# Optimization experiments

Measured on AMD Instinct MI355X. Metric: run time of the kernel, lower is better.

Reference implementation:

```python
import jax, jax.numpy as jnp
import numpy as np

B, S, D = 4, 2048, 1024
H, K = 16, 64
EPS = 1e-3  # Keras LayerNormalization default epsilon


def setup_inputs() -> dict:
    key = jax.random.key(0)
    ks = jax.random.split(key, 11)
    s = 0.02
    return {
        "x":  jax.random.normal(ks[0], (B, S, D), jnp.float32),
        "Wq": jax.random.normal(ks[1], (D, H, K), jnp.float32) * s,
        "bq": jnp.zeros((H, K), jnp.float32),
        "Wk": jax.random.normal(ks[2], (D, H, K), jnp.float32) * s,
        "bk": jnp.zeros((H, K), jnp.float32),
        "Wv": jax.random.normal(ks[3], (D, H, K), jnp.float32) * s,
        "bv": jnp.zeros((H, K), jnp.float32),
        "Wo": jax.random.normal(ks[4], (H, K, D), jnp.float32) * s,
        "bo": jnp.zeros((D,), jnp.float32),
        "gamma": jnp.ones((D,), jnp.float32),
        "beta":  jnp.zeros((D,), jnp.float32),
    }


def reference(x, Wq, bq, Wk, bk, Wv, bv, Wo, bo, gamma, beta):
    # QKV projections (Keras MHA einsum form): [B,S,D] -> [B,S,H,K]
    q = jnp.einsum("bsd,dhk->bshk", x, Wq) + bq
    k = jnp.einsum("bsd,dhk->bshk", x, Wk) + bk
    v = jnp.einsum("bsd,dhk->bshk", x, Wv) + bv
    scale = 1.0 / jnp.sqrt(jnp.asarray(K, x.dtype))
    scores = jnp.einsum("bqhk,bshk->bhqs", q, k) * scale  # [B,H,S,S]
    attn = jax.nn.softmax(scores, axis=-1)
    ctx = jnp.einsum("bhqs,bshk->bqhk", attn, v)           # [B,S,H,K]
    attn_out = jnp.einsum("bqhk,hkd->bqd", ctx, Wo) + bo   # [B,S,D]
    # residual + LayerNorm (over last axis)
    y = x + attn_out
    mu = jnp.mean(y, axis=-1, keepdims=True)
    var = jnp.mean(jnp.square(y - mu), axis=-1, keepdims=True)
    return (y - mu) * jax.lax.rsqrt(var + EPS) * gamma + beta
```

## Files before the change

kernel.cpp:

```cpp
#include <hip/hip_runtime.h>

typedef float f32x4 __attribute__((ext_vector_type(4)));
typedef float f32x16 __attribute__((ext_vector_type(16)));
typedef __bf16 bf16x8 __attribute__((ext_vector_type(8)));
typedef __bf16 bf16x4 __attribute__((ext_vector_type(4)));
typedef __bf16 bf16x2 __attribute__((ext_vector_type(2)));
typedef unsigned short us4 __attribute__((ext_vector_type(4)));

#define DEV __device__ __forceinline__

DEV unsigned short f2bf(float f) {
  union { float f; unsigned int u; } v; v.f = f;
  unsigned int u = v.u;
  return (unsigned short)((u + 0x7FFFu + ((u >> 16) & 1u)) >> 16);
}

typedef const __attribute__((address_space(1))) void* gvp;
typedef __attribute__((address_space(3))) void* lvp;

DEV void gll16(const void* g, void* l) {
  __builtin_amdgcn_global_load_lds((gvp)g, (lvp)l, 16, 0, 0);
}

DEV float fexp2(float x) { return __builtin_amdgcn_exp2f(x); }

DEV void plswap(unsigned& a, unsigned& b) {
  asm("v_permlane32_swap_b32 %0, %1" : "+v"(a), "+v"(b));
}
DEV float xhalf_max(float v) {
  union { float f; unsigned u; } a, b;
  a.f = v; b.f = v;
  plswap(a.u, b.u);
  return fmaxf(a.f, b.f);
}
DEV float xhalf_sum(float v) {
  union { float f; unsigned u; } a, b;
  a.f = v; b.f = v;
  plswap(a.u, b.u);
  return a.f + b.f;
}

__global__ void k_convert(const float* __restrict__ in, unsigned short* __restrict__ out, int n4) {
  int i = blockIdx.x * blockDim.x + threadIdx.x;
  if (i < n4) {
    float4 v = ((const float4*)in)[i];
    us4 o = { f2bf(v.x), f2bf(v.y), f2bf(v.z), f2bf(v.w) };
    ((us4*)out)[i] = o;
  }
}

__global__ void k_transpose4(const float* __restrict__ w0, const float* __restrict__ w1,
                             const float* __restrict__ w2, const float* __restrict__ w3,
                             unsigned short* __restrict__ o0, unsigned short* __restrict__ o1,
                             unsigned short* __restrict__ o2, unsigned short* __restrict__ o3) {
  const float* in = (blockIdx.z == 0) ? w0 : (blockIdx.z == 1) ? w1 : (blockIdx.z == 2) ? w2 : w3;
  unsigned short* out = (blockIdx.z == 0) ? o0 : (blockIdx.z == 1) ? o1 : (blockIdx.z == 2) ? o2 : o3;
  __shared__ float tile[32][33];
  const int bx = blockIdx.x * 32, by = blockIdx.y * 32;
  const int tx = threadIdx.x, ty = threadIdx.y;
#pragma unroll
  for (int r = 0; r < 4; ++r)
    tile[ty + r * 8][tx] = in[(size_t)(by + ty + r * 8) * 1024 + bx + tx];
  __syncthreads();
#pragma unroll
  for (int r = 0; r < 4; ++r)
    out[(size_t)(bx + ty + r * 8) * 1024 + by + tx] = f2bf(tile[tx][ty + r * 8]);
}

template<int MODE>
__global__ void k_gemm(const unsigned short* __restrict__ A,
                       const unsigned short* __restrict__ Bt,
                       const float* __restrict__ bias,
                       void* __restrict__ outp,
                       const float* __restrict__ xres,
                       int Kd, float scale) {
  __shared__ unsigned short As[128 * 64];
  __shared__ unsigned short Bs[128 * 64];
  const int tid = threadIdx.x;
  const int lane = tid & 63;
  const int wave = tid >> 6;
  const int l15 = lane & 15;
  const int lq  = lane >> 4;
  const int wm = wave >> 1, wn = wave & 1;
  const int mbase = blockIdx.x * 128;
  const int nbase = blockIdx.y * 128;

  f32x4 acc[4][4] = {};

  for (int kt = 0; kt < Kd; kt += 64) {
    __syncthreads();
#pragma unroll
    for (int c = 0; c < 4; ++c) {
      int e = (c * 256 + tid) * 8;
      int row = e >> 6;
      int o2 = (e * 2) ^ ((row & 7) << 4);
      int col = (o2 >> 1) & 63;
      gll16(A + (size_t)(mbase + row) * Kd + kt + col,
            As + (c * 256 + (tid & ~63)) * 8);
    }
#pragma unroll
    for (int c = 0; c < 4; ++c) {
      int e = (c * 256 + tid) * 8;
      int row = e >> 6;
      int o2 = (e * 2) ^ ((row & 7) << 4);
      int col = (o2 >> 1) & 63;
      gll16(Bt + (size_t)(nbase + row) * Kd + kt + col,
            Bs + (c * 256 + (tid & ~63)) * 8);
    }
    __syncthreads();
#pragma unroll
    for (int ks = 0; ks < 2; ++ks) {
      bf16x8 af[4], bfv[4];
#pragma unroll
      for (int i = 0; i < 4; ++i) {
        int row = wm * 64 + i * 16 + l15;
        int off = row * 128 + ((((ks << 2) | lq) ^ (row & 7)) << 4);
        af[i] = *(const bf16x8*)((const char*)As + off);
      }
#pragma unroll
      for (int j = 0; j < 4; ++j) {
        int row = wn * 64 + j * 16 + l15;
        int off = row * 128 + ((((ks << 2) | lq) ^ (row & 7)) << 4);
        bfv[j] = *(const bf16x8*)((const char*)Bs + off);
      }
#pragma unroll
      for (int i = 0; i < 4; ++i)
#pragma unroll
        for (int j = 0; j < 4; ++j)
          acc[i][j] = __builtin_amdgcn_mfma_f32_16x16x32_bf16(af[i], bfv[j], acc[i][j], 0, 0, 0);
    }
  }

#pragma unroll
  for (int i = 0; i < 4; ++i) {
#pragma unroll
    for (int j = 0; j < 4; ++j) {
#pragma unroll
      for (int r = 0; r < 4; ++r) {
        int mi = mbase + wm * 64 + i * 16 + lq * 4 + r;
        int nj = nbase + wn * 64 + j * 16 + l15;
        float v = acc[i][j][r];
        if constexpr (MODE == 0) {
          v = (v + bias[nj]) * scale;
          int b = mi >> 11, s = mi & 2047, h = nj >> 6, kk = nj & 63;
          ((unsigned short*)outp)[(((size_t)((b << 4) + h) * 2048 + s) << 6) + kk] = f2bf(v);
        } else if constexpr (MODE == 1) {
          v = v + bias[mi];
          int h = mi >> 6, d = mi & 63, b = nj >> 11, s = nj & 2047;
          ((unsigned short*)outp)[(((size_t)((b << 4) + h) << 6) + d) * 2048 + s] = f2bf(v);
        } else {
          size_t idx = (size_t)mi * 1024 + nj;
          ((float*)outp)[idx] = v + bias[nj] + xres[idx];
        }
      }
    }
  }
}

__global__ __launch_bounds__(256, 4) void k_attn(const unsigned short* __restrict__ q,
                       const unsigned short* __restrict__ k,
                       const unsigned short* __restrict__ vt,
                       unsigned short* __restrict__ ctx) {
  __shared__ unsigned short KV[2][2][64 * 64];

  const int tid = threadIdx.x;
  const int lane = tid & 63;
  const int wave = tid >> 6;
  const int l31 = lane & 31;
  const int l5 = lane >> 5;

  const int bid = blockIdx.x;
  const int swz = (bid & 7) * 128 + (bid >> 3);
  const int bh = swz >> 4;
  const int qtile = swz & 15;
  const int qbase = qtile * 128;
  const size_t sl = (size_t)bh << 17;

  const int qrow = qbase + wave * 32 + l31;
  bf16x8 qreg[4];
#pragma unroll
  for (int ds = 0; ds < 4; ++ds)
    qreg[ds] = *(const bf16x8*)(q + sl + (size_t)qrow * 64 + ds * 16 + l5 * 8);

#define STAGE_KV(BUF, TT) do {                                                 \
    const int kvb_ = (TT) * 64;                                                \
    _Pragma("unroll")                                                          \
    for (int c = 0; c < 2; ++c) {                                              \
      int e = (c * 256 + tid) * 8;                                             \
      int row_ = e >> 6;                                                       \
      int o2 = (e * 2) ^ ((row_ & 7) << 4);                                    \
      int col_ = (o2 >> 1) & 63;                                               \
      gll16(k + sl + (size_t)(kvb_ + row_) * 64 + col_,                        \
            KV[BUF][0] + (c * 256 + (tid & ~63)) * 8);                         \
      gll16(vt + sl + (size_t)row_ * 2048 + kvb_ + col_,                       \
            KV[BUF][1] + (c * 256 + (tid & ~63)) * 8);                         \
    }                                                                          \
  } while (0)

  STAGE_KV(0, 0);
  __syncthreads();

  f32x16 acc0 = {}, acc1 = {};
  float mrow = -1e30f, lrow = 0.f;

  for (int t = 0; t < 32; ++t) {
    const int cur = t & 1;
    if (t < 31) STAGE_KV(cur ^ 1, t + 1);

    const char* Ksc = (const char*)KV[cur][0];
    const char* Vtc = (const char*)KV[cur][1];

    f32x16 st0 = {}, st1 = {};
    __builtin_amdgcn_s_setprio(1);
#pragma unroll
    for (int kvh = 0; kvh < 2; ++kvh) {
      bf16x8 kf[4];
#pragma unroll
      for (int ds = 0; ds < 4; ++ds) {
        int row = kvh * 32 + l31;
        kf[ds] = *(const bf16x8*)(Ksc + row * 128 + (((ds * 32 + l5 * 16)) ^ ((row & 7) << 4)));
      }
      if (kvh == 0) {
#pragma unroll
        for (int ds = 0; ds < 4; ++ds)
          st0 = __builtin_amdgcn_mfma_f32_32x32x16_bf16(kf[ds], qreg[ds], st0, 0, 0, 0);
      } else {
#pragma unroll
        for (int ds = 0; ds < 4; ++ds)
          st1 = __builtin_amdgcn_mfma_f32_32x32x16_bf16(kf[ds], qreg[ds], st1, 0, 0, 0);
      }
    }
    __builtin_amdgcn_s_setprio(0);

    float tmax[8];
#pragma unroll
    for (int i = 0; i < 8; ++i) tmax[i] = fmaxf(st0[i], st0[i + 8]);
#pragma unroll
    for (int i = 0; i < 8; ++i) tmax[i] = fmaxf(tmax[i], fmaxf(st1[i], st1[i + 8]));
    float tm = fmaxf(fmaxf(fmaxf(tmax[0], tmax[1]), fmaxf(tmax[2], tmax[3])),
                     fmaxf(fmaxf(tmax[4], tmax[5]), fmaxf(tmax[6], tmax[7])));
    tm = xhalf_max(tm);

    if (!__all(tm <= mrow + 10.0f)) {
      float mnew = fmaxf(mrow, tm);
      float alpha = fexp2(mrow - mnew);
      acc0 *= alpha;
      acc1 *= alpha;
      lrow *= alpha;
      mrow = mnew;
    }
    const float mc = mrow;

    unsigned pk0[8], pk1[8];
    float rs0 = 0.f, rs1 = 0.f, rs2 = 0.f, rs3 = 0.f;
#pragma unroll
    for (int m = 0; m < 8; ++m) {
      float a0 = fexp2(st0[2 * m] - mc), a1 = fexp2(st0[2 * m + 1] - mc);
      float b0 = fexp2(st1[2 * m] - mc), b1 = fexp2(st1[2 * m + 1] - mc);
      rs0 += a0; rs1 += a1; rs2 += b0; rs3 += b1;
      union { bf16x2 v; unsigned u; } ua, ub;
      ua.v = bf16x2{ (__bf16)a0, (__bf16)a1 };
      ub.v = bf16x2{ (__bf16)b0, (__bf16)b1 };
      pk0[m] = ua.u; pk1[m] = ub.u;
    }
    lrow += (rs0 + rs1) + (rs2 + rs3);

    bf16x8 av[2][4];
#pragma unroll
    for (int kvg = 0; kvg < 4; ++kvg)
#pragma unroll
      for (int dh = 0; dh < 2; ++dh) {
        int row = dh * 32 + l31;
        av[dh][kvg] = *(const bf16x8*)(Vtc + row * 128 + ((kvg * 32 + l5 * 16) ^ ((row & 7) << 4)));
      }

    union PF { unsigned u[4]; bf16x8 v; };
    PF pf[2][2];
#pragma unroll
    for (int kvh = 0; kvh < 2; ++kvh) {
      unsigned* pk = kvh ? pk1 : pk0;
#pragma unroll
      for (int g = 0; g < 2; ++g)
#pragma unroll
        for (int j = 0; j < 2; ++j) {
          unsigned a = pk[4 * g + j], b = pk[4 * g + 2 + j];
          plswap(a, b);
          pf[kvh][g].u[j] = a;
          pf[kvh][g].u[2 + j] = b;
        }
    }

    __builtin_amdgcn_s_setprio(1);
#pragma unroll
    for (int kvh = 0; kvh < 2; ++kvh)
#pragma unroll
      for (int g = 0; g < 2; ++g) {
        const int kvg = 2 * kvh + g;
        acc0 = __builtin_amdgcn_mfma_f32_32x32x16_bf16(av[0][kvg], pf[kvh][g].v, acc0, 0, 0, 0);
        acc1 = __builtin_amdgcn_mfma_f32_32x32x16_bf16(av[1][kvg], pf[kvh][g].v, acc1, 0, 0, 0);
      }
    __builtin_amdgcn_s_setprio(0);

    __syncthreads();
  }

  float inv = 1.f / xhalf_sum(lrow);

  unsigned short* TR = (unsigned short*)KV;
  const int qloc = wave * 32 + l31;
  const int swq = (qloc & 7) << 4;
#pragma unroll
  for (int dh = 0; dh < 2; ++dh) {
    const f32x16& ac = dh ? acc1 : acc0;
#pragma unroll
    for (int g3 = 0; g3 < 4; ++g3) {
      bf16x4 o4 = { (__bf16)(ac[4 * g3] * inv), (__bf16)(ac[4 * g3 + 1] * inv),
                    (__bf16)(ac[4 * g3 + 2] * inv), (__bf16)(ac[4 * g3 + 3] * inv) };
      *(bf16x4*)((char*)TR + qloc * 128 + ((dh * 64 + g3 * 16 + l5 * 8) ^ swq)) = o4;
    }
  }
  __syncthreads();

  const int b = bh >> 4, h = bh & 15;
  {
    int row = tid >> 1, half = tid & 1;
    int sw = (row & 7) << 4;
    unsigned short* gdst = ctx + (size_t)(b * 2048 + qbase + row) * 1024 + h * 64 + half * 32;
#pragma unroll
    for (int i = 0; i < 4; ++i) {
      bf16x8 vv = *(const bf16x8*)((const char*)TR + row * 128 + ((half * 64 + i * 16) ^ sw));
      *(bf16x8*)(gdst + i * 8) = vv;
    }
  }
#undef STAGE_KV
}

__global__ void k_ln(const float* __restrict__ y, const float* __restrict__ gamma,
                     const float* __restrict__ beta, float* __restrict__ out) {
  const int row = blockIdx.x;
  const int tid = threadIdx.x;
  const float4 v = ((const float4*)(y + (size_t)row * 1024))[tid];
  float sum = v.x + v.y + v.z + v.w;
  float sq = v.x * v.x + v.y * v.y + v.z * v.z + v.w * v.w;
#pragma unroll
  for (int m = 1; m <= 32; m <<= 1) {
    sum += __shfl_xor(sum, m);
    sq  += __shfl_xor(sq, m);
  }
  __shared__ float s1[4], s2[4];
  const int wv = tid >> 6, lane = tid & 63;
  if (lane == 0) { s1[wv] = sum; s2[wv] = sq; }
  __syncthreads();
  sum = s1[0] + s1[1] + s1[2] + s1[3];
  sq  = s2[0] + s2[1] + s2[2] + s2[3];
  const float mu = sum * (1.f / 1024.f);
  const float rs = rsqrtf(sq * (1.f / 1024.f) - mu * mu + 1e-3f);
  const float4 g  = ((const float4*)gamma)[tid];
  const float4 bb = ((const float4*)beta)[tid];
  float4 o;
  o.x = (v.x - mu) * rs * g.x + bb.x;
  o.y = (v.y - mu) * rs * g.y + bb.y;
  o.z = (v.z - mu) * rs * g.z + bb.z;
  o.w = (v.w - mu) * rs * g.w + bb.w;
  ((float4*)(out + (size_t)row * 1024))[tid] = o;
}

extern "C" void kernel_launch(void* const* d_in, const int* in_sizes, int n_in,
                              void* d_out, int out_size, void* d_ws, size_t ws_size,
                              hipStream_t stream) {
  const float* x  = (const float*)d_in[0];
  const float* Wq = (const float*)d_in[1];
  const float* bq = (const float*)d_in[2];
  const float* Wk = (const float*)d_in[3];
  const float* bk = (const float*)d_in[4];
  const float* Wv = (const float*)d_in[5];
  const float* bv = (const float*)d_in[6];
  const float* Wo = (const float*)d_in[7];
  const float* bo = (const float*)d_in[8];
  const float* gamma = (const float*)d_in[9];
  const float* beta  = (const float*)d_in[10];
  float* out = (float*)d_out;

  char* ws = (char*)d_ws;
  const size_t MB = 1024 * 1024;
  unsigned short* xb  = (unsigned short*)(ws);
  unsigned short* wqt = (unsigned short*)(ws + 16 * MB);
  unsigned short* wkt = (unsigned short*)(ws + 18 * MB);
  unsigned short* wvt = (unsigned short*)(ws + 20 * MB);
  unsigned short* wot = (unsigned short*)(ws + 22 * MB);
  unsigned short* qb  = (unsigned short*)(ws + 24 * MB);
  unsigned short* kb  = (unsigned short*)(ws + 40 * MB);
  unsigned short* vtb = (unsigned short*)(ws + 56 * MB);
  unsigned short* ctx = (unsigned short*)(ws + 72 * MB);
  float* yb = (float*)(ws + 24 * MB);

  k_convert<<<8192, 256, 0, stream>>>(x, xb, 2097152);
  dim3 tb(32, 8), tg(32, 32, 4);
  k_transpose4<<<tg, tb, 0, stream>>>(Wq, Wk, Wv, Wo, wqt, wkt, wvt, wot);

  k_gemm<0><<<dim3(64, 8), 256, 0, stream>>>(xb, wqt, bq, qb, nullptr, 1024, 0.18033688011112042f);
  k_gemm<0><<<dim3(64, 8), 256, 0, stream>>>(xb, wkt, bk, kb, nullptr, 1024, 1.0f);
  k_gemm<1><<<dim3(8, 64), 256, 0, stream>>>(wvt, xb, bv, vtb, nullptr, 1024, 1.0f);

  k_attn<<<1024, 256, 0, stream>>>(qb, kb, vtb, ctx);

  k_gemm<2><<<dim3(64, 8), 256, 0, stream>>>(ctx, wot, bo, yb, x, 1024, 1.0f);

  k_ln<<<8192, 256, 0, stream>>>(yb, gamma, beta, out);
  (void)in_sizes; (void)n_in; (void)out_size; (void)ws_size;
}
```

Measured before the change: 208.0 us.

## Double attention query tile per block and merge QKV GEMMs into one launch

The attention kernel now handles 256 query rows per block, with each wave owning two 32-row query groups that share the same K/V fragments loaded from LDS. This halves the K/V global and LDS traffic per query and halves the grid to 512 blocks. The cost is more registers per wave, so launch bounds drop to 2 blocks per SM. Separately, the Q, K and V projection GEMMs are fused into one launch using blockIdx.z, which removes two kernel launches and lets the three GEMMs run concurrently.

After: 206.6 us. No clear change (-0.6%).

```diff
diff --git a/kernel.cpp b/kernel.cpp
--- a/kernel.cpp
+++ b/kernel.cpp
@@ -67,13 +67,101 @@
     out[(size_t)(bx + ty + r * 8) * 1024 + by + tx] = f2bf(tile[tx][ty + r * 8]);
 }
 
-template<int MODE>
-__global__ void k_gemm(const unsigned short* __restrict__ A,
-                       const unsigned short* __restrict__ Bt,
-                       const float* __restrict__ bias,
-                       void* __restrict__ outp,
-                       const float* __restrict__ xres,
-                       int Kd, float scale) {
+__global__ void k_gemm_qkv(const unsigned short* __restrict__ xb,
+                           const unsigned short* __restrict__ wqt,
+                           const unsigned short* __restrict__ wkt,
+                           const unsigned short* __restrict__ wvt,
+                           const float* __restrict__ bq, const float* __restrict__ bk,
+                           const float* __restrict__ bv,
+                           unsigned short* __restrict__ qb, unsigned short* __restrict__ kb,
+                           unsigned short* __restrict__ vtb) {
+  __shared__ unsigned short As[128 * 64];
+  __shared__ unsigned short Bs[128 * 64];
+  const int tid = threadIdx.x;
+  const int lane = tid & 63;
+  const int wave = tid >> 6;
+  const int l15 = lane & 15;
+  const int lq  = lane >> 4;
+  const int wm = wave >> 1, wn = wave & 1;
+  const int z = blockIdx.z;
+
+  const unsigned short* A;
+  const unsigned short* Bt;
+  int mbase, nbase;
+  if (z == 2) { A = wvt; Bt = xb; mbase = blockIdx.y * 128; nbase = blockIdx.x * 128; }
+  else        { A = xb; Bt = z ? wkt : wqt; mbase = blockIdx.x * 128; nbase = blockIdx.y * 128; }
+
+  f32x4 acc[4][4] = {};
+
+  for (int kt = 0; kt < 1024; kt += 64) {
+    __syncthreads();
+#pragma unroll
+    for (int c = 0; c < 4; ++c) {
+      int e = (c * 256 + tid) * 8;
+      int row = e >> 6;
+      int o2 = (e * 2) ^ ((row & 7) << 4);
+      int col = (o2 >> 1) & 63;
+      gll16(A + (size_t)(mbase + row) * 1024 + kt + col,
+            As + (c * 256 + (tid & ~63)) * 8);
+      gll16(Bt + (size_t)(nbase + row) * 1024 + kt + col,
+            Bs + (c * 256 + (tid & ~63)) * 8);
+    }
+    __syncthreads();
+#pragma unroll
+    for (int ks = 0; ks < 2; ++ks) {
+      bf16x8 af[4], bfv[4];
+#pragma unroll
+      for (int i = 0; i < 4; ++i) {
+        int row = wm * 64 + i * 16 + l15;
+        int off = row * 128 + ((((ks << 2) | lq) ^ (row & 7)) << 4);
+        af[i] = *(const bf16x8*)((const char*)As + off);
+      }
+#pragma unroll
+      for (int j = 0; j < 4; ++j) {
+        int row = wn * 64 + j * 16 + l15;
+        int off = row * 128 + ((((ks << 2) | lq) ^ (row & 7)) << 4);
+        bfv[j] = *(const bf16x8*)((const char*)Bs + off);
+      }
+#pragma unroll
+      for (int i = 0; i < 4; ++i)
+#pragma unroll
+        for (int j = 0; j < 4; ++j)
+          acc[i][j] = __builtin_amdgcn_mfma_f32_16x16x32_bf16(af[i], bfv[j], acc[i][j], 0, 0, 0);
+    }
+  }
+
+  const float scale = (z == 0) ? 0.18033688011112042f : 1.0f;
+  const float* bias = (z == 0) ? bq : (z == 1) ? bk : bv;
+  unsigned short* outp = (z == 0) ? qb : (z == 1) ? kb : vtb;
+
+#pragma unroll
+  for (int i = 0; i < 4; ++i) {
+#pragma unroll
+    for (int j = 0; j < 4; ++j) {
+#pragma unroll
+      for (int r = 0; r < 4; ++r) {
+        int mi = mbase + wm * 64 + i * 16 + lq * 4 + r;
+        int nj = nbase + wn * 64 + j * 16 + l15;
+        float v = acc[i][j][r];
+        if (z < 2) {
+          v = (v + bias[nj]) * scale;
+          int b = mi >> 11, s = mi & 2047, h = nj >> 6, kk = nj & 63;
+          outp[(((size_t)((b << 4) + h) * 2048 + s) << 6) + kk] = f2bf(v);
+        } else {
+          v = v + bias[mi];
+          int h = mi >> 6, d = mi & 63, b = nj >> 11, s = nj & 2047;
+          outp[(((size_t)((b << 4) + h) << 6) + d) * 2048 + s] = f2bf(v);
+        }
+      }
+    }
+  }
+}
+
+__global__ void k_gemm_out(const unsigned short* __restrict__ A,
+                           const unsigned short* __restrict__ Bt,
+                           const float* __restrict__ bias,
+                           float* __restrict__ outp,
+                           const float* __restrict__ xres) {
   __shared__ unsigned short As[128 * 64];
   __shared__ unsigned short Bs[128 * 64];
   const int tid = threadIdx.x;
@@ -87,7 +175,7 @@
 
   f32x4 acc[4][4] = {};
 
-  for (int kt = 0; kt < Kd; kt += 64) {
+  for (int kt = 0; kt < 1024; kt += 64) {
     __syncthreads();
 #pragma unroll
     for (int c = 0; c < 4; ++c) {
@@ -95,16 +183,9 @@
       int row = e >> 6;
       int o2 = (e * 2) ^ ((row & 7) << 4);
       int col = (o2 >> 1) & 63;
-      gll16(A + (size_t)(mbase + row) * Kd + kt + col,
+      gll16(A + (size_t)(mbase + row) * 1024 + kt + col,
             As + (c * 256 + (tid & ~63)) * 8);
-    }
-#pragma unroll
-    for (int c = 0; c < 4; ++c) {
-      int e = (c * 256 + tid) * 8;
-      int row = e >> 6;
-      int o2 = (e * 2) ^ ((row & 7) << 4);
-      int col = (o2 >> 1) & 63;
-      gll16(Bt + (size_t)(nbase + row) * Kd + kt + col,
+      gll16(Bt + (size_t)(nbase + row) * 1024 + kt + col,
             Bs + (c * 256 + (tid & ~63)) * 8);
     }
     __syncthreads();
@@ -132,32 +213,19 @@
   }
 
 #pragma unroll
-  for (int i = 0; i < 4; ++i) {
-#pragma unroll
-    for (int j = 0; j < 4; ++j) {
+  for (int i = 0; i < 4; ++i)
+#pragma unroll
+    for (int j = 0; j < 4; ++j)
 #pragma unroll
       for (int r = 0; r < 4; ++r) {
         int mi = mbase + wm * 64 + i * 16 + lq * 4 + r;
         int nj = nbase + wn * 64 + j * 16 + l15;
-        float v = acc[i][j][r];
-        if constexpr (MODE == 0) {
-          v = (v + bias[nj]) * scale;
-          int b = mi >> 11, s = mi & 2047, h = nj >> 6, kk = nj & 63;
-          ((unsigned short*)outp)[(((size_t)((b << 4) + h) * 2048 + s) << 6) + kk] = f2bf(v);
-        } else if constexpr (MODE == 1) {
-          v = v + bias[mi];
-          int h = mi >> 6, d = mi & 63, b = nj >> 11, s = nj & 2047;
-          ((unsigned short*)outp)[(((size_t)((b << 4) + h) << 6) + d) * 2048 + s] = f2bf(v);
-        } else {
-          size_t idx = (size_t)mi * 1024 + nj;
-          ((float*)outp)[idx] = v + bias[nj] + xres[idx];
-        }
-      }
-    }
-  }
-}
-
-__global__ __launch_bounds__(256, 4) void k_attn(const unsigned short* __restrict__ q,
+        size_t idx = (size_t)mi * 1024 + nj;
+        outp[idx] = acc[i][j][r] + bias[nj] + xres[idx];
+      }
+}
+
+__global__ __launch_bounds__(256, 2) void k_attn(const unsigned short* __restrict__ q,
                        const unsigned short* __restrict__ k,
                        const unsigned short* __restrict__ vt,
                        unsigned short* __restrict__ ctx) {
@@ -170,17 +238,22 @@
   const int l5 = lane >> 5;
 
   const int bid = blockIdx.x;
-  const int swz = (bid & 7) * 128 + (bid >> 3);
-  const int bh = swz >> 4;
-  const int qtile = swz & 15;
-  const int qbase = qtile * 128;
+  const int swz = (bid & 7) * 64 + (bid >> 3);
+  const int bh = swz >> 3;
+  const int qtile = swz & 7;
+  const int qbase = qtile * 256;
   const size_t sl = (size_t)bh << 17;
 
-  const int qrow = qbase + wave * 32 + l31;
-  bf16x8 qreg[4];
-#pragma unroll
-  for (int ds = 0; ds < 4; ++ds)
-    qreg[ds] = *(const bf16x8*)(q + sl + (size_t)qrow * 64 + ds * 16 + l5 * 8);
+  bf16x8 qrA[4], qrB[4];
+  {
+    const int qrowA = qbase + wave * 64 + l31;
+    const int qrowB = qrowA + 32;
+#pragma unroll
+    for (int ds = 0; ds < 4; ++ds) {
+      qrA[ds] = *(const bf16x8*)(q + sl + (size_t)qrowA * 64 + ds * 16 + l5 * 8);
+      qrB[ds] = *(const bf16x8*)(q + sl + (size_t)qrowB * 64 + ds * 16 + l5 * 8);
+    }
+  }
 
 #define STAGE_KV(BUF, TT) do {                                                 \
     const int kvb_ = (TT) * 64;                                                \
@@ -200,8 +273,63 @@
   STAGE_KV(0, 0);
   __syncthreads();
 
-  f32x16 acc0 = {}, acc1 = {};
-  float mrow = -1e30f, lrow = 0.f;
+  f32x16 accA0 = {}, accA1 = {}, accB0 = {}, accB1 = {};
+  float mrA = -1e30f, lrA = 0.f, mrB = -1e30f, lrB = 0.f;
+  unsigned pkA0[8], pkA1[8], pkB0[8], pkB1[8];
+
+#define QK_SOFTMAX(QR, A0, A1, MR, LR, P0, P1) do {                            \
+    f32x16 s0 = {}, s1 = {};                                                   \
+    __builtin_amdgcn_s_setprio(1);                                             \
+    _Pragma("unroll") for (int ds = 0; ds < 4; ++ds)                           \
+      s0 = __builtin_amdgcn_mfma_f32_32x32x16_bf16(kf0[ds], QR[ds], s0, 0,0,0);\
+    _Pragma("unroll") for (int ds = 0; ds < 4; ++ds)                           \
+      s1 = __builtin_amdgcn_mfma_f32_32x32x16_bf16(kf1[ds], QR[ds], s1, 0,0,0);\
+    __builtin_amdgcn_s_setprio(0);                                             \
+    float tmax[8];                                                             \
+    _Pragma("unroll") for (int i = 0; i < 8; ++i)                              \
+      tmax[i] = fmaxf(s0[i], s0[i + 8]);                                       \
+    _Pragma("unroll") for (int i = 0; i < 8; ++i)                              \
+      tmax[i] = fmaxf(tmax[i], fmaxf(s1[i], s1[i + 8]));                       \
+    float tm = fmaxf(fmaxf(fmaxf(tmax[0], tmax[1]), fmaxf(tmax[2], tmax[3])),  \
+                     fmaxf(fmaxf(tmax[4], tmax[5]), fmaxf(tmax[6], tmax[7]))); \
+    tm = xhalf_max(tm);                                                        \
+    if (!__all(tm <= MR + 10.0f)) {                                            \
+      float mnew = fmaxf(MR, tm);                                              \
+      float alpha = fexp2(MR - mnew);                                          \
+      A0 *= alpha; A1 *= alpha; LR *= alpha; MR = mnew;                        \
+    }                                                                          \
+    const float mc_ = MR;                                                      \
+    float r0 = 0.f, r1 = 0.f, r2 = 0.f, r3 = 0.f;                              \
+    _Pragma("unroll") for (int m = 0; m < 8; ++m) {                            \
+      float a0 = fexp2(s0[2*m] - mc_), a1 = fexp2(s0[2*m+1] - mc_);            \
+      float b0 = fexp2(s1[2*m] - mc_), b1 = fexp2(s1[2*m+1] - mc_);            \
+      r0 += a0; r1 += a1; r2 += b0; r3 += b1;                                  \
+      union { bf16x2 v; unsigned u; } ua, ub;                                  \
+      ua.v = bf16x2{ (__bf16)a0, (__bf16)a1 };                                 \
+      ub.v = bf16x2{ (__bf16)b0, (__bf16)b1 };                                 \
+      P0[m] = ua.u; P1[m] = ub.u;                                              \
+    }                                                                          \
+    LR += (r0 + r1) + (r2 + r3);                                               \
+  } while (0)
+
+#define PV_STEP(P0, P1, A0, A1) do {                                           \
+    _Pragma("unroll") for (int kvh = 0; kvh < 2; ++kvh) {                      \
+      unsigned* pk_ = kvh ? (P1) : (P0);                                       \
+      _Pragma("unroll") for (int g = 0; g < 2; ++g) {                          \
+        unsigned a0_ = pk_[4*g],     b0_ = pk_[4*g + 2];                       \
+        unsigned a1_ = pk_[4*g + 1], b1_ = pk_[4*g + 3];                       \
+        plswap(a0_, b0_);                                                      \
+        plswap(a1_, b1_);                                                      \
+        union { unsigned u[4]; bf16x8 v; } pf;                                 \
+        pf.u[0] = a0_; pf.u[1] = a1_; pf.u[2] = b0_; pf.u[3] = b1_;            \
+        const int kvg = 2 * kvh + g;                                           \
+        __builtin_amdgcn_s_setprio(1);                                         \
+        A0 = __builtin_amdgcn_mfma_f32_32x32x16_bf16(av0[kvg], pf.v, A0, 0,0,0);\
+        A1 = __builtin_amdgcn_mfma_f32_32x32x16_bf16(av1[kvg], pf.v, A1, 0,0,0);\
+        __builtin_amdgcn_s_setprio(0);                                         \
+      }                                                                        \
+    }                                                                          \
+  } while (0)
 
   for (int t = 0; t < 32; ++t) {
     const int cur = t & 1;
@@ -210,120 +338,56 @@
     const char* Ksc = (const char*)KV[cur][0];
     const char* Vtc = (const char*)KV[cur][1];
 
-    f32x16 st0 = {}, st1 = {};
-    __builtin_amdgcn_s_setprio(1);
-#pragma unroll
-    for (int kvh = 0; kvh < 2; ++kvh) {
-      bf16x8 kf[4];
-#pragma unroll
-      for (int ds = 0; ds < 4; ++ds) {
-        int row = kvh * 32 + l31;
-        kf[ds] = *(const bf16x8*)(Ksc + row * 128 + (((ds * 32 + l5 * 16)) ^ ((row & 7) << 4)));
-      }
-      if (kvh == 0) {
-#pragma unroll
-        for (int ds = 0; ds < 4; ++ds)
-          st0 = __builtin_amdgcn_mfma_f32_32x32x16_bf16(kf[ds], qreg[ds], st0, 0, 0, 0);
-      } else {
-#pragma unroll
-        for (int ds = 0; ds < 4; ++ds)
-          st1 = __builtin_amdgcn_mfma_f32_32x32x16_bf16(kf[ds], qreg[ds], st1, 0, 0, 0);
-      }
-    }
-    __builtin_amdgcn_s_setprio(0);
-
-    float tmax[8];
-#pragma unroll
-    for (int i = 0; i < 8; ++i) tmax[i] = fmaxf(st0[i], st0[i + 8]);
-#pragma unroll
-    for (int i = 0; i < 8; ++i) tmax[i] = fmaxf(tmax[i], fmaxf(st1[i], st1[i + 8]));
-    float tm = fmaxf(fmaxf(fmaxf(tmax[0], tmax[1]), fmaxf(tmax[2], tmax[3])),
-                     fmaxf(fmaxf(tmax[4], tmax[5]), fmaxf(tmax[6], tmax[7])));
-    tm = xhalf_max(tm);
-
-    if (!__all(tm <= mrow + 10.0f)) {
-      float mnew = fmaxf(mrow, tm);
-      float alpha = fexp2(mrow - mnew);
-      acc0 *= alpha;
-      acc1 *= alpha;
-      lrow *= alpha;
-      mrow = mnew;
-    }
-    const float mc = mrow;
-
-    unsigned pk0[8], pk1[8];
-    float rs0 = 0.f, rs1 = 0.f, rs2 = 0.f, rs3 = 0.f;
-#pragma unroll
-    for (int m = 0; m < 8; ++m) {
-      float a0 = fexp2(st0[2 * m] - mc), a1 = fexp2(st0[2 * m + 1] - mc);
-      float b0 = fexp2(st1[2 * m] - mc), b1 = fexp2(st1[2 * m + 1] - mc);
-      rs0 += a0; rs1 += a1; rs2 += b0; rs3 += b1;
-      union { bf16x2 v; unsigned u; } ua, ub;
-      ua.v = bf16x2{ (__bf16)a0, (__bf16)a1 };
-      ub.v = bf16x2{ (__bf16)b0, (__bf16)b1 };
-      pk0[m] = ua.u; pk1[m] = ub.u;
-    }
-    lrow += (rs0 + rs1) + (rs2 + rs3);
-
-    bf16x8 av[2][4];
-#pragma unroll
-    for (int kvg = 0; kvg < 4; ++kvg)
-#pragma unroll
-      for (int dh = 0; dh < 2; ++dh) {
-        int row = dh * 32 + l31;
-        av[dh][kvg] = *(const bf16x8*)(Vtc + row * 128 + ((kvg * 32 + l5 * 16) ^ ((row & 7) << 4)));
-      }
-
-    union PF { unsigned u[4]; bf16x8 v; };
-    PF pf[2][2];
-#pragma unroll
-    for (int kvh = 0; kvh < 2; ++kvh) {
-      unsigned* pk = kvh ? pk1 : pk0;
-#pragma unroll
-      for (int g = 0; g < 2; ++g)
-#pragma unroll
-        for (int j = 0; j < 2; ++j) {
-          unsigned a = pk[4 * g + j], b = pk[4 * g + 2 + j];
-          plswap(a, b);
-          pf[kvh][g].u[j] = a;
-          pf[kvh][g].u[2 + j] = b;
-        }
-    }
-
-    __builtin_amdgcn_s_setprio(1);
-#pragma unroll
-    for (int kvh = 0; kvh < 2; ++kvh)
-#pragma unroll
-      for (int g = 0; g < 2; ++g) {
-        const int kvg = 2 * kvh + g;
-        acc0 = __builtin_amdgcn_mfma_f32_32x32x16_bf16(av[0][kvg], pf[kvh][g].v, acc0, 0, 0, 0);
-        acc1 = __builtin_amdgcn_mfma_f32_32x32x16_bf16(av[1][kvg], pf[kvh][g].v, acc1, 0, 0, 0);
-      }
-    __builtin_amdgcn_s_setprio(0);
+    bf16x8 kf0[4], kf1[4];
+#pragma unroll
+    for (int ds = 0; ds < 4; ++ds) {
+      int r0 = l31, r1 = 32 + l31;
+      kf0[ds] = *(const bf16x8*)(Ksc + r0 * 128 + ((ds * 32 + l5 * 16) ^ ((r0 & 7) << 4)));
+      kf1[ds] = *(const bf16x8*)(Ksc + r1 * 128 + ((ds * 32 + l5 * 16) ^ ((r1 & 7) << 4)));
+    }
+
+    QK_SOFTMAX(qrA, accA0, accA1, mrA, lrA, pkA0, pkA1);
+    QK_SOFTMAX(qrB, accB0, accB1, mrB, lrB, pkB0, pkB1);
+
+    bf16x8 av0[4], av1[4];
+#pragma unroll
+    for (int kvg = 0; kvg < 4; ++kvg) {
+      int r0 = l31, r1 = 32 + l31;
+      av0[kvg] = *(const bf16x8*)(Vtc + r0 * 128 + ((kvg * 32 + l5 * 16) ^ ((r0 & 7) << 4)));
+      av1[kvg] = *(const bf16x8*)(Vtc + r1 * 128 + ((kvg * 32 + l5 * 16) ^ ((r1 & 7) << 4)));
+    }
+
+    PV_STEP(pkA0, pkA1, accA0, accA1);
+    PV_STEP(pkB0, pkB1, accB0, accB1);
 
     __syncthreads();
   }
 
-  float inv = 1.f / xhalf_sum(lrow);
+  const float invA = 1.f / xhalf_sum(lrA);
+  const float invB = 1.f / xhalf_sum(lrB);
 
   unsigned short* TR = (unsigned short*)KV;
-  const int qloc = wave * 32 + l31;
-  const int swq = (qloc & 7) << 4;
-#pragma unroll
-  for (int dh = 0; dh < 2; ++dh) {
-    const f32x16& ac = dh ? acc1 : acc0;
-#pragma unroll
-    for (int g3 = 0; g3 < 4; ++g3) {
-      bf16x4 o4 = { (__bf16)(ac[4 * g3] * inv), (__bf16)(ac[4 * g3 + 1] * inv),
-                    (__bf16)(ac[4 * g3 + 2] * inv), (__bf16)(ac[4 * g3 + 3] * inv) };
-      *(bf16x4*)((char*)TR + qloc * 128 + ((dh * 64 + g3 * 16 + l5 * 8) ^ swq)) = o4;
-    }
-  }
+#define WRITE_O(ACC0, ACC1, INV, QG) do {                                      \
+    const int qloc = wave * 64 + (QG) * 32 + l31;                              \
+    const int swq = (qloc & 7) << 4;                                           \
+    _Pragma("unroll") for (int dh = 0; dh < 2; ++dh) {                         \
+      const f32x16& ac = dh ? (ACC1) : (ACC0);                                 \
+      _Pragma("unroll") for (int g3 = 0; g3 < 4; ++g3) {                       \
+        bf16x4 o4 = { (__bf16)(ac[4*g3] * (INV)),  (__bf16)(ac[4*g3+1] * (INV)), \
+                      (__bf16)(ac[4*g3+2] * (INV)),(__bf16)(ac[4*g3+3] * (INV)) }; \
+        *(bf16x4*)((char*)TR + qloc * 128 + ((dh * 64 + g3 * 16 + l5 * 8) ^ swq)) = o4; \
+      }                                                                        \
+    }                                                                          \
+  } while (0)
+
+  WRITE_O(accA0, accA1, invA, 0);
+  WRITE_O(accB0, accB1, invB, 1);
   __syncthreads();
 
   const int b = bh >> 4, h = bh & 15;
-  {
-    int row = tid >> 1, half = tid & 1;
+#pragma unroll
+  for (int pass = 0; pass < 2; ++pass) {
+    int row = pass * 128 + (tid >> 1), half = tid & 1;
     int sw = (row & 7) << 4;
     unsigned short* gdst = ctx + (size_t)(b * 2048 + qbase + row) * 1024 + h * 64 + half * 32;
 #pragma unroll
@@ -333,6 +397,9 @@
     }
   }
 #undef STAGE_KV
+#undef QK_SOFTMAX
+#undef PV_STEP
+#undef WRITE_O
 }
 
 __global__ void k_ln(const float* __restrict__ y, const float* __restrict__ gamma,
@@ -398,13 +465,11 @@
   dim3 tb(32, 8), tg(32, 32, 4);
   k_transpose4<<<tg, tb, 0, stream>>>(Wq, Wk, Wv, Wo, wqt, wkt, wvt, wot);
 
-  k_gemm<0><<<dim3(64, 8), 256, 0, stream>>>(xb, wqt, bq, qb, nullptr, 1024, 0.18033688011112042f);
-  k_gemm<0><<<dim3(64, 8), 256, 0, stream>>>(xb, wkt, bk, kb, nullptr, 1024, 1.0f);
-  k_gemm<1><<<dim3(8, 64), 256, 0, stream>>>(wvt, xb, bv, vtb, nullptr, 1024, 1.0f);
-
-  k_attn<<<1024, 256, 0, stream>>>(qb, kb, vtb, ctx);
-
-  k_gemm<2><<<dim3(64, 8), 256, 0, stream>>>(ctx, wot, bo, yb, x, 1024, 1.0f);
+  k_gemm_qkv<<<dim3(64, 8, 3), 256, 0, stream>>>(xb, wqt, wkt, wvt, bq, bk, bv, qb, kb, vtb);
+
+  k_attn<<<512, 256, 0, stream>>>(qb, kb, vtb, ctx);
+
+  k_gemm_out<<<dim3(64, 8), 256, 0, stream>>>(ctx, wot, bo, yb, x);
 
   k_ln<<<8192, 256, 0, stream>>>(yb, gamma, beta, out);
   (void)in_sizes; (void)n_in; (void)out_size; (void)ws_size;
```
